# Performance work log

Hardware: AMD Instinct MI355X
Metric: run time of the kernel (lower is better)

The kernel has to match this reference:

```python
import jax, jax.numpy as jnp
import numpy as np

B, S, D = 16, 2048, 128

def setup_inputs() -> dict:
    key = jax.random.key(0)
    kq, kk, kv, km = jax.random.split(key, 4)
    Q = jax.random.normal(kq, (B, S, D), dtype=jnp.float32)
    K = jax.random.normal(kk, (B, S, D), dtype=jnp.float32)
    V = jax.random.normal(kv, (B, S, D), dtype=jnp.float32)
    # mask: True entries are masked out (filled with -inf), same as torch.masked_fill_
    mask = jax.random.randint(km, (B, S, S), 0, 2).astype(bool)
    return {"Q": Q, "K": K, "V": V, "mask": mask, "dk": 128}

def reference(Q, K, V, mask, dk):
    # scores: [B, S_q, S_k]
    w = jnp.einsum('bqd,bkd->bqk', Q, K)
    w = jnp.where(mask, -jnp.inf, w)
    # scale applied to masked scores (as in original: mask first, then divide);
    # -inf / scale stays -inf, so math matches exactly.
    scale = jnp.asarray(dk, w.dtype) ** 0.5
    p = jax.nn.softmax(w / scale, axis=-1)
    # context: [B, S_q, D]
    return jnp.einsum('bqk,bkd->bqd', p, V)
```

## Files before the change

kernel.cpp:

```cpp
#include <hip/hip_runtime.h>
#include <hip/hip_bf16.h>
#include <stdint.h>

typedef __attribute__((ext_vector_type(8)))  short short8;
typedef __attribute__((ext_vector_type(4)))  float floatx4;
typedef __attribute__((ext_vector_type(16))) float floatx16;

#define S_LEN 2048
#define DH    128
#define BQ    64
#define BKV   64
#define NSTEP (S_LEN / BKV)
#define SCALE 0.08838834764831845f
#define SCALE2 0.12753785429791905f
#define DTHR 11.541560327111708f

__device__ __forceinline__ float ex2(float x) { return __builtin_amdgcn_exp2f(x); }

__device__ __forceinline__ unsigned short f2b(float f) {
    union { float f; unsigned u; } v; v.f = f;
    unsigned r = v.u + 0x7fffu + ((v.u >> 16) & 1u);
    return (unsigned short)(r >> 16);
}

__device__ __forceinline__ unsigned cvt_pk(float lo, float hi) {
    unsigned r;
    asm("v_cvt_pk_bf16_f32 %0, %1, %2" : "=v"(r) : "v"(lo), "v"(hi));
    return r;
}

__device__ __forceinline__ void gll16(const void* g, void* l) {
    __builtin_amdgcn_global_load_lds(
        (__attribute__((address_space(1))) void*)(g),
        (__attribute__((address_space(3))) void*)(l), 16, 0, 0);
}


__global__ __launch_bounds__(256) void conv_k(const float* __restrict__ K,
                                              unsigned short* __restrict__ Kbf)
{
    int i = blockIdx.x * 256 + threadIdx.x;
    float4 v = ((const float4*)K)[i];
    ushort4 o;
    o.x = f2b(v.x); o.y = f2b(v.y); o.z = f2b(v.z); o.w = f2b(v.w);
    ((ushort4*)Kbf)[i] = o;
}

__global__ __launch_bounds__(256) void transp_v(const float* __restrict__ V,
                                                unsigned short* __restrict__ Vt)
{
    __shared__ float t[32][33];
    const int k0 = blockIdx.x * 32, d0 = blockIdx.y * 32, b = blockIdx.z;
    const int tx = threadIdx.x & 31, ty = threadIdx.x >> 5;
    const float* Vb = V + ((size_t)b * S_LEN + k0) * DH + d0;
    #pragma unroll
    for (int i = 0; i < 4; ++i)
        t[ty + 8 * i][tx] = Vb[(size_t)(ty + 8 * i) * DH + tx];
    __syncthreads();
    unsigned short* Vtb = Vt + ((size_t)b * DH + d0) * S_LEN + k0;
    #pragma unroll
    for (int i = 0; i < 4; ++i)
        Vtb[(size_t)(ty + 8 * i) * S_LEN + tx] = f2b(t[tx][ty + 8 * i]);
}

#define LDS_BYTES 69632

__global__ __launch_bounds__(256, 2)
void attn_fwd(const float* __restrict__ Q, const unsigned short* __restrict__ Kbf,
              const unsigned short* __restrict__ Vt, const int* __restrict__ M,
              float* __restrict__ O)
{
    __shared__ __align__(128) char lds[LDS_BYTES];

    const int tid  = threadIdx.x;
    const int lane = tid & 63;
    const int w    = tid >> 6;
    const int wq   = w & 1;
    const int wk   = w >> 1;
    const int lq   = lane & 31;
    const int hi   = lane >> 5;
    const int qt   = blockIdx.x;
    const int b    = blockIdx.y;
    const int q0   = qt * BQ;

    const int vd = tid & 127;
    const int vh = tid >> 7;
    const int krow_l = lane >> 4;
    const int kcol_l = (lane & 15) * 16;

    short8 qf[8];
    {
        const float* qrow = Q + ((size_t)(b * S_LEN + q0 + wq * 32 + lq)) * DH;
        #pragma unroll
        for (int dsub = 0; dsub < 8; ++dsub) {
            const float* p = qrow + dsub * 16 + hi * 8;
            float4 a  = *(const float4*)(p);
            float4 bb = *(const float4*)(p + 4);
            short8 f;
            f[0] = f2b(a.x * SCALE2);  f[1] = f2b(a.y * SCALE2);
            f[2] = f2b(a.z * SCALE2);  f[3] = f2b(a.w * SCALE2);
            f[4] = f2b(bb.x * SCALE2); f[5] = f2b(bb.y * SCALE2);
            f[6] = f2b(bb.z * SCALE2); f[7] = f2b(bb.w * SCALE2);
            qf[dsub] = f;
        }
    }

    float m_run = -1e30f;
    float l_run = 0.f;
    floatx16 accO[4];
    #pragma unroll
    for (int i = 0; i < 4; ++i) accO[i] = (floatx16)(0.f);

    const char*           Kb8 = (const char*)(Kbf + (size_t)b * S_LEN * DH);
    const unsigned short* Vtb = Vt + (size_t)b * DH * S_LEN;
    const int* Mrow = M + (size_t)b * S_LEN * S_LEN
                        + (size_t)(q0 + wq * 32 + lq) * S_LEN + wk * 32 + 4 * hi;

    short8 vreg[4];
    int4   mcur[4];

#define LOAD_MASK(TT) {                                                       \
    const int* mp_ = Mrow + (TT) * BKV;                                       \
    mcur[0] = *(const int4*)(mp_);                                            \
    mcur[1] = *(const int4*)(mp_ + 8);                                        \
    mcur[2] = *(const int4*)(mp_ + 16);                                       \
    mcur[3] = *(const int4*)(mp_ + 24); }

    #pragma unroll
    for (int i = 0; i < 4; ++i) {
        int j = (w << 2) | i;
        int r = 4 * j + krow_l;
        unsigned cb = (unsigned)kcol_l ^ (unsigned)((r & 15) << 4);
        gll16(Kb8 + (size_t)r * 256 + cb, lds + j * 1024);
    }
    #pragma unroll
    for (int j = 0; j < 4; ++j)
        vreg[j] = *(const short8*)(Vtb + (size_t)vd * S_LEN + vh * 32 + j * 8);
    #pragma unroll
    for (int j = 0; j < 4; ++j)
        *(short8*)(lds + 32768 + vd * 144 + vh * 64 + j * 16) = vreg[j];
    #pragma unroll
    for (int j = 0; j < 4; ++j)
        vreg[j] = *(const short8*)(Vtb + (size_t)vd * S_LEN + BKV + vh * 32 + j * 8);
    LOAD_MASK(0);
    __syncthreads();

#define STEP_BODY(T) {                                                        \
    const int pb  = (T) & 1;                                                  \
    const int kv0 = (T) * BKV;                                                \
                                                  \
    if ((T) + 1 < NSTEP) {                                                    \
        const char* Ksrc = Kb8 + (size_t)(kv0 + BKV) * 256;                   \
        char* KHn = lds + ((pb ^ 1) * 16384);                                 \
        _Pragma("unroll")                                                     \
        for (int i = 0; i < 4; ++i) {                                         \
            int j = (w << 2) | i;                                             \
            int r = 4 * j + krow_l;                                           \
            unsigned cb = (unsigned)kcol_l ^ (unsigned)((r & 15) << 4);       \
            gll16(Ksrc + (size_t)r * 256 + cb, KHn + j * 1024);               \
        }                                                                     \
    }                                                                         \
                            \
    if ((T) + 1 < NSTEP) {                                                    \
        _Pragma("unroll")                                                     \
        for (int j = 0; j < 4; ++j)                                           \
            *(short8*)(lds + 32768 + (pb ^ 1) * 18432 + vd * 144 + vh * 64    \
                       + j * 16) = vreg[j];                                   \
    }                                                                         \
    if ((T) + 2 < NSTEP) {                                                    \
        const unsigned short* vs_ = Vtb + (size_t)vd * S_LEN                  \
                                   + (kv0 + 2 * BKV) + vh * 32;               \
        _Pragma("unroll")                                                     \
        for (int j = 0; j < 4; ++j)                                           \
            vreg[j] = *(const short8*)(vs_ + j * 8);                          \
    }                                                                         \
            \
    floatx16 accS = (floatx16)(0.f);                                          \
    {                                                                         \
        const char* KHp = lds + pb * 16384;                                   \
        const int krow = wk * 32 + lq;                                        \
        const char* kbase = KHp + krow * 256;                                 \
        const unsigned ksw = (unsigned)((krow & 15) << 4);                    \
        __builtin_amdgcn_s_setprio(1);                                        \
        _Pragma("unroll")                                                     \
        for (int dsub = 0; dsub < 8; ++dsub) {                                \
            short8 kf = *(const short8*)(kbase +                              \
                ((unsigned)(dsub * 32 + hi * 16) ^ ksw));                     \
            accS = __builtin_amdgcn_mfma_f32_32x32x16_bf16(                   \
                       kf, qf[dsub], accS, 0, 0, 0);                          \
        }                                                                     \
        __builtin_amdgcn_s_setprio(0);                                        \
    }                                                                         \
      \
    float p_[16];                                                             \
    _Pragma("unroll")                                                         \
    for (int j = 0; j < 4; ++j) {                                             \
        int4 mm = mcur[j];                                                    \
        p_[4*j+0] = mm.x ? -1e30f : accS[4*j+0];                              \
        p_[4*j+1] = mm.y ? -1e30f : accS[4*j+1];                              \
        p_[4*j+2] = mm.z ? -1e30f : accS[4*j+2];                              \
        p_[4*j+3] = mm.w ? -1e30f : accS[4*j+3];                              \
    }                                                                         \
    float mx = p_[0];                                                         \
    _Pragma("unroll")                                                         \
    for (int r = 1; r < 16; ++r) mx = fmaxf(mx, p_[r]);                       \
    mx = fmaxf(mx, __shfl_xor(mx, 32));                                       \
    int need = __any(mx - m_run > DTHR);                                      \
    float corr = 1.0f;                                                        \
    if (need) {                                                               \
        float mn = fmaxf(m_run, mx);                                          \
        corr = ex2(m_run - mn);                                               \
        m_run = mn;                                                           \
    }                                                                         \
    float ts = 0.f;                                                           \
    _Pragma("unroll")                                                         \
    for (int r = 0; r < 16; ++r) { p_[r] = ex2(p_[r] - m_run); ts += p_[r]; } \
    ts += __shfl_xor(ts, 32);                                                 \
    if (need) {                                                               \
        l_run = l_run * corr + ts;                                            \
        _Pragma("unroll")                                                     \
        for (int ds = 0; ds < 4; ++ds) {                                      \
            floatx16 o = accO[ds];                                            \
            _Pragma("unroll")                                                 \
            for (int r = 0; r < 16; ++r) o[r] *= corr;                        \
            accO[ds] = o;                                                     \
        }                                                                     \
    } else {                                                                  \
        l_run += ts;                                                          \
    }                                                                         \
    if ((T) + 1 < NSTEP) LOAD_MASK((T) + 1);                                  \
              \
    short8 pf[2];                                                             \
    _Pragma("unroll")                                                         \
    for (int ks = 0; ks < 2; ++ks) {                                          \
        unsigned a01 = cvt_pk(p_[8*ks+0], p_[8*ks+1]);                        \
        unsigned a23 = cvt_pk(p_[8*ks+2], p_[8*ks+3]);                        \
        unsigned b01 = cvt_pk(p_[8*ks+4], p_[8*ks+5]);                        \
        unsigned b23 = cvt_pk(p_[8*ks+6], p_[8*ks+7]);                        \
        unsigned ta01 = (unsigned)__shfl_xor((int)a01, 32);                   \
        unsigned ta23 = (unsigned)__shfl_xor((int)a23, 32);                   \
        unsigned tb01 = (unsigned)__shfl_xor((int)b01, 32);                   \
        unsigned tb23 = (unsigned)__shfl_xor((int)b23, 32);                   \
        union { unsigned u[4]; short8 v; } pu;                                \
        pu.u[0] = hi ? tb01 : a01;                                            \
        pu.u[1] = hi ? tb23 : a23;                                            \
        pu.u[2] = hi ? b01 : ta01;                                            \
        pu.u[3] = hi ? b23 : ta23;                                            \
        pf[ks] = pu.v;                                                        \
    }                                                                         \
           \
    {                                                                         \
        const char* VTp = lds + 32768 + pb * 18432;                           \
        __builtin_amdgcn_s_setprio(1);                                        \
        _Pragma("unroll")                                                     \
        for (int ds = 0; ds < 4; ++ds) {                                      \
            const char* vbase = VTp + (ds * 32 + lq) * 144 + wk * 64 + hi*16; \
            _Pragma("unroll")                                                 \
            for (int ks = 0; ks < 2; ++ks) {                                  \
                short8 vf = *(const short8*)(vbase + ks * 32);                \
                accO[ds] = __builtin_amdgcn_mfma_f32_32x32x16_bf16(           \
                               vf, pf[ks], accO[ds], 0, 0, 0);                \
            }                                                                 \
        }                                                                     \
        __builtin_amdgcn_s_setprio(0);                                        \
    }                                                                         \
    __syncthreads(); }

    for (int t = 0; t < NSTEP; ++t) {
        STEP_BODY(t)
    }
#undef STEP_BODY
#undef LOAD_MASK

    {
        float* mg = (float*)lds;
        const int slot = (wq * 64 + lane) * 68;
        if (wk == 1) {
            #pragma unroll
            for (int ds = 0; ds < 4; ++ds)
                #pragma unroll
                for (int rr = 0; rr < 4; ++rr) {
                    float4 v;
                    v.x = accO[ds][4*rr+0]; v.y = accO[ds][4*rr+1];
                    v.z = accO[ds][4*rr+2]; v.w = accO[ds][4*rr+3];
                    *(float4*)(mg + slot + ds * 16 + rr * 4) = v;
                }
            mg[slot + 64] = m_run;
            mg[slot + 65] = l_run;
        }
        __syncthreads();
        if (wk == 0) {
            float m1 = mg[slot + 64], l1 = mg[slot + 65];
            float m  = fmaxf(m_run, m1);
            float f0 = ex2(m_run - m), f1 = ex2(m1 - m);
            float l  = l_run * f0 + l1 * f1;
            float inv = (l > 0.f) ? 1.f / l : 0.f;
            float* Ob = O + ((size_t)(b * S_LEN + q0 + wq * 32 + lq)) * DH;
            #pragma unroll
            for (int ds = 0; ds < 4; ++ds)
                #pragma unroll
                for (int rr = 0; rr < 4; ++rr) {
                    float4 part = *(const float4*)(mg + slot + ds * 16 + rr * 4);
                    float4 ov;
                    ov.x = (accO[ds][4*rr+0] * f0 + part.x * f1) * inv;
                    ov.y = (accO[ds][4*rr+1] * f0 + part.y * f1) * inv;
                    ov.z = (accO[ds][4*rr+2] * f0 + part.z * f1) * inv;
                    ov.w = (accO[ds][4*rr+3] * f0 + part.w * f1) * inv;
                    *(float4*)(Ob + ds * 32 + 8 * rr + 4 * hi) = ov;
                }
        }
    }
}

#define FB_LDS_BYTES 77824

__global__ __launch_bounds__(256, 2)
void attn_fwd_fb(const float* __restrict__ Q, const float* __restrict__ K,
                 const float* __restrict__ V, const int* __restrict__ M,
                 float* __restrict__ O)
{
    __shared__ __align__(128) char lds[FB_LDS_BYTES];

    const int tid  = threadIdx.x;
    const int lane = tid & 63;
    const int w    = tid >> 6;
    const int c    = lane & 15;
    const int g    = lane >> 4;
    const int qt   = blockIdx.x;
    const int b    = blockIdx.y;
    const int q0   = qt * 64;

    const int rbase = tid >> 5;
    const int c4    = tid & 31;
    const unsigned swk = (unsigned)(c4 * 8) ^ (unsigned)(rbase << 4);
    const int vd    = tid & 127;
    const int vk0   = (tid >> 7) * 32;

    short8 qf[4];
    {
        const float* qrow = Q + ((size_t)(b * S_LEN + q0 + w * 16 + c)) * DH;
        #pragma unroll
        for (int dk = 0; dk < 4; ++dk) {
            const float* p = qrow + dk * 32 + g * 8;
            float4 a  = *(const float4*)(p);
            float4 bb = *(const float4*)(p + 4);
            short8 f;
            f[0] = f2b(a.x * SCALE);  f[1] = f2b(a.y * SCALE);
            f[2] = f2b(a.z * SCALE);  f[3] = f2b(a.w * SCALE);
            f[4] = f2b(bb.x * SCALE); f[5] = f2b(bb.y * SCALE);
            f[6] = f2b(bb.z * SCALE); f[7] = f2b(bb.w * SCALE);
            qf[dk] = f;
        }
    }

    float m_run[4] = {-1e30f, -1e30f, -1e30f, -1e30f};
    float l_run[4] = {0.f, 0.f, 0.f, 0.f};
    floatx4 accO[8];
    #pragma unroll
    for (int i = 0; i < 8; ++i) accO[i] = (floatx4)(0.f);

    const float* Kb = K + (size_t)b * S_LEN * DH;
    const float* Vb = V + (size_t)b * S_LEN * DH;
    const int*   Mb = M + (size_t)b * S_LEN * S_LEN + (size_t)q0 * S_LEN;

    size_t moff[4];
    #pragma unroll
    for (int r = 0; r < 4; ++r)
        moff[r] = (size_t)(w * 16 + 4 * g + r) * S_LEN;

    float4 kreg[8];
    float  vreg[32];
    int    mreg[16];

    #pragma unroll
    for (int i = 0; i < 8; ++i)
        kreg[i] = *(const float4*)(Kb + (size_t)(i * 8 + rbase) * DH + c4 * 4);
    #pragma unroll
    for (int j = 0; j < 32; ++j)
        vreg[j] = Vb[(size_t)(vk0 + j) * DH + vd];
    #pragma unroll
    for (int r = 0; r < 4; ++r)
        #pragma unroll
        for (int n = 0; n < 4; ++n)
            mreg[r * 4 + n] = Mb[moff[r] + n * 16 + c];

    #pragma unroll
    for (int i = 0; i < 8; ++i) {
        float4 kv = kreg[i];
        unsigned long long kp =
              (unsigned long long)f2b(kv.x)
            | ((unsigned long long)f2b(kv.y) << 16)
            | ((unsigned long long)f2b(kv.z) << 32)
            | ((unsigned long long)f2b(kv.w) << 48);
        *(unsigned long long*)(lds + (i * 8 + rbase) * 256 + swk) = kp;
    }
    {
        char* vbase = lds + 32768 + vd * 144 + vk0 * 2;
        #pragma unroll
        for (int i = 0; i < 4; ++i) {
            short8 pk;
            #pragma unroll
            for (int e = 0; e < 8; ++e) pk[e] = f2b(vreg[i * 8 + e]);
            *(short8*)(vbase + i * 16) = pk;
        }
    }
    #pragma unroll
    for (int i = 0; i < 8; ++i)
        kreg[i] = *(const float4*)(Kb + (size_t)(BKV + i * 8 + rbase) * DH + c4 * 4);
    #pragma unroll
    for (int j = 0; j < 32; ++j)
        vreg[j] = Vb[(size_t)(BKV + vk0 + j) * DH + vd];

    __syncthreads();

    char* psw = lds + 69632 + w * 2048;

    for (int step = 0; step < NSTEP; ++step) {
        const int p = step & 1;
        const int kv0 = step * BKV;
        char* KHp = lds + p * 16384;
        char* VTp = lds + 32768 + p * 18432;

        floatx4 accS[4];
        #pragma unroll
        for (int n = 0; n < 4; ++n) accS[n] = (floatx4)(0.f);
        #pragma unroll
        for (int n = 0; n < 4; ++n) {
            const char* krow = KHp + (n * 16 + c) * 256;
            #pragma unroll
            for (int dk = 0; dk < 4; ++dk) {
                unsigned colb = (unsigned)(dk * 64 + g * 16) ^ (unsigned)((c & 7) << 4);
                short8 kf = *(const short8*)(krow + colb);
                accS[n] = __builtin_amdgcn_mfma_f32_16x16x32_bf16(qf[dk], kf, accS[n], 0, 0, 0);
            }
        }

        float pv[4][4];
        float corr[4];
        #pragma unroll
        for (int r = 0; r < 4; ++r) {
            float sv[4];
            #pragma unroll
            for (int n = 0; n < 4; ++n) {
                float s = accS[n][r];
                if (mreg[r * 4 + n]) s = -1e30f;
                sv[n] = s;
            }
            float tm = fmaxf(fmaxf(sv[0], sv[1]), fmaxf(sv[2], sv[3]));
            #pragma unroll
            for (int off = 1; off < 16; off <<= 1)
                tm = fmaxf(tm, __shfl_xor(tm, off, 64));
            float mn = fmaxf(m_run[r], tm);
            corr[r]  = __expf(m_run[r] - mn);
            m_run[r] = mn;
            float ts = 0.f;
            #pragma unroll
            for (int n = 0; n < 4; ++n) { pv[n][r] = __expf(sv[n] - mn); ts += pv[n][r]; }
            #pragma unroll
            for (int off = 1; off < 16; off <<= 1)
                ts += __shfl_xor(ts, off, 64);
            l_run[r] = l_run[r] * corr[r] + ts;
        }
        if (step + 1 < NSTEP) {
            const int kvn = kv0 + BKV;
            #pragma unroll
            for (int r = 0; r < 4; ++r)
                #pragma unroll
                for (int n = 0; n < 4; ++n)
                    mreg[r * 4 + n] = Mb[moff[r] + kvn + n * 16 + c];
        }

        #pragma unroll
        for (int s8 = 0; s8 < 8; ++s8) {
            floatx4 o = accO[s8];
            o[0] *= corr[0]; o[1] *= corr[1]; o[2] *= corr[2]; o[3] *= corr[3];
            accO[s8] = o;
        }

        #pragma unroll
        for (int r = 0; r < 4; ++r) {
            int rl = 4 * g + r;
            #pragma unroll
            for (int n = 0; n < 4; ++n) {
                unsigned colb = (unsigned)((n * 16 + c) * 2) ^ (unsigned)((rl & 7) << 4);
                *(unsigned short*)(psw + rl * 128 + colb) = f2b(pv[n][r]);
            }
        }

        #pragma unroll
        for (int sub = 0; sub < 2; ++sub) {
            unsigned colb = (unsigned)(sub * 64 + g * 16) ^ (unsigned)((c & 7) << 4);
            short8 pf = *(const short8*)(psw + c * 128 + colb);
            #pragma unroll
            for (int s8 = 0; s8 < 8; ++s8) {
                short8 vf = *(const short8*)(VTp + (s8 * 16 + c) * 144 + sub * 64 + g * 16);
                accO[s8] = __builtin_amdgcn_mfma_f32_16x16x32_bf16(pf, vf, accO[s8], 0, 0, 0);
            }
        }

        if (step + 1 < NSTEP) {
            char* KHn = lds + (p ^ 1) * 16384;
            char* VTn = lds + 32768 + (p ^ 1) * 18432;
            #pragma unroll
            for (int i = 0; i < 8; ++i) {
                float4 kv = kreg[i];
                unsigned long long kp =
                      (unsigned long long)f2b(kv.x)
                    | ((unsigned long long)f2b(kv.y) << 16)
                    | ((unsigned long long)f2b(kv.z) << 32)
                    | ((unsigned long long)f2b(kv.w) << 48);
                *(unsigned long long*)(KHn + (i * 8 + rbase) * 256 + swk) = kp;
            }
            char* vbase = VTn + vd * 144 + vk0 * 2;
            #pragma unroll
            for (int i = 0; i < 4; ++i) {
                short8 pk;
                #pragma unroll
                for (int e = 0; e < 8; ++e) pk[e] = f2b(vreg[i * 8 + e]);
                *(short8*)(vbase + i * 16) = pk;
            }
            if (step + 2 < NSTEP) {
                const int kvn2 = kv0 + 2 * BKV;
                #pragma unroll
                for (int i = 0; i < 8; ++i)
                    kreg[i] = *(const float4*)(Kb + (size_t)(kvn2 + i * 8 + rbase) * DH + c4 * 4);
                #pragma unroll
                for (int j = 0; j < 32; ++j)
                    vreg[j] = Vb[(size_t)(kvn2 + vk0 + j) * DH + vd];
            }
        }
        __syncthreads();
    }

    float inv[4];
    #pragma unroll
    for (int r = 0; r < 4; ++r) inv[r] = (l_run[r] > 0.f) ? 1.f / l_run[r] : 0.f;
    float* Ob = O + ((size_t)(b * S_LEN + q0 + w * 16)) * DH;
    #pragma unroll
    for (int s8 = 0; s8 < 8; ++s8) {
        #pragma unroll
        for (int r = 0; r < 4; ++r) {
            Ob[(size_t)(4 * g + r) * DH + s8 * 16 + c] = accO[s8][r] * inv[r];
        }
    }
}

extern "C" void kernel_launch(void* const* d_in, const int* in_sizes, int n_in,
                              void* d_out, int out_size, void* d_ws, size_t ws_size,
                              hipStream_t stream) {
    const float* Q = (const float*)d_in[0];
    const float* K = (const float*)d_in[1];
    const float* V = (const float*)d_in[2];
    const int*   M = (const int*)d_in[3];
    float*       O = (float*)d_out;

    const size_t elems = (size_t)16 * S_LEN * DH;
    if (ws_size >= 2 * elems * sizeof(unsigned short)) {
        unsigned short* Kbf = (unsigned short*)d_ws;
        unsigned short* Vt  = (unsigned short*)d_ws + elems;
        conv_k<<<dim3((unsigned)(elems / 4 / 256)), dim3(256), 0, stream>>>(K, Kbf);
        transp_v<<<dim3(S_LEN / 32, DH / 32, 16), dim3(256), 0, stream>>>(V, Vt);
        attn_fwd<<<dim3(S_LEN / BQ, 16), dim3(256), 0, stream>>>(Q, Kbf, Vt, M, O);
    } else {
        attn_fwd_fb<<<dim3(S_LEN / 64, 16), dim3(256), 0, stream>>>(Q, K, V, M, O);
    }
}
```

Before: 118.5 us.

## Pre-pack attention mask into bitmasks via ballot before the attention kernel

Adds a pack_mask kernel that reads the int32 mask once and uses wave ballots to compress it into 64-bit bitmasks, 32 words per query row. The attention kernel then reads those bitmasks instead of 16-byte int vectors per step, and double-buffers one group of four KV steps ahead. This cuts the mask traffic and register pressure inside the compute-bound attention loop. The cost is an extra kernel launch and serialising the full mask read ahead of attention instead of overlapping it. It also needs more workspace, and the slow fallback path runs if that workspace is missing.

```diff
diff --git a/kernel.cpp b/kernel.cpp
--- a/kernel.cpp
+++ b/kernel.cpp
@@ -63,11 +63,36 @@
         Vtb[(size_t)(ty + 8 * i) * S_LEN + tx] = f2b(t[tx][ty + 8 * i]);
 }
 
+__global__ __launch_bounds__(256) void pack_mask(const int* __restrict__ M,
+                                                 unsigned long long* __restrict__ P)
+{
+    const int lane = threadIdx.x & 63;
+    const int wv   = threadIdx.x >> 6;
+    const int row  = blockIdx.x * 4 + wv;
+    const int* Mr  = M + (size_t)row * S_LEN;
+    unsigned long long* Pr = P + (size_t)row * 32;
+    #pragma unroll
+    for (int it = 0; it < 8; ++it) {
+        int4 v = *(const int4*)(Mr + it * 256 + lane * 4);
+        unsigned long long b0 = __ballot(v.x != 0);
+        unsigned long long b1 = __ballot(v.y != 0);
+        unsigned long long b2 = __ballot(v.z != 0);
+        unsigned long long b3 = __ballot(v.w != 0);
+        if (lane == 0) {
+            Pr[it * 4 + 0] = b0;
+            Pr[it * 4 + 1] = b1;
+            Pr[it * 4 + 2] = b2;
+            Pr[it * 4 + 3] = b3;
+        }
+    }
+}
+
 #define LDS_BYTES 69632
 
 __global__ __launch_bounds__(256, 2)
 void attn_fwd(const float* __restrict__ Q, const unsigned short* __restrict__ Kbf,
-              const unsigned short* __restrict__ Vt, const int* __restrict__ M,
+              const unsigned short* __restrict__ Vt,
+              const unsigned long long* __restrict__ Pm,
               float* __restrict__ O)
 {
     __shared__ __align__(128) char lds[LDS_BYTES];
@@ -113,18 +138,16 @@
 
     const char*           Kb8 = (const char*)(Kbf + (size_t)b * S_LEN * DH);
     const unsigned short* Vtb = Vt + (size_t)b * DH * S_LEN;
-    const int* Mrow = M + (size_t)b * S_LEN * S_LEN
-                        + (size_t)(q0 + wq * 32 + lq) * S_LEN + wk * 32 + 4 * hi;
+    const unsigned long long* Pk = Pm
+        + ((size_t)(b * S_LEN + q0 + wq * 32 + lq) << 5);
 
     short8 vreg[4];
-    int4   mcur[4];
-
-#define LOAD_MASK(TT) {                                                       \
-    const int* mp_ = Mrow + (TT) * BKV;                                       \
-    mcur[0] = *(const int4*)(mp_);                                            \
-    mcur[1] = *(const int4*)(mp_ + 8);                                        \
-    mcur[2] = *(const int4*)(mp_ + 16);                                       \
-    mcur[3] = *(const int4*)(mp_ + 24); }
+    unsigned long long mgc[4], mgn[4];
+
+#define LOAD_MG(DST, G) {                                                     \
+    ulonglong2 a_ = *(const ulonglong2*)(Pk + (G) * 4);                       \
+    ulonglong2 b_ = *(const ulonglong2*)(Pk + (G) * 4 + 2);                   \
+    DST[0] = a_.x; DST[1] = a_.y; DST[2] = b_.x; DST[3] = b_.y; }
 
     #pragma unroll
     for (int i = 0; i < 4; ++i) {
@@ -142,10 +165,11 @@
     #pragma unroll
     for (int j = 0; j < 4; ++j)
         vreg[j] = *(const short8*)(Vtb + (size_t)vd * S_LEN + BKV + vh * 32 + j * 8);
-    LOAD_MASK(0);
+    LOAD_MG(mgc, 0);
+    LOAD_MG(mgn, 1);
     __syncthreads();
 
-#define STEP_BODY(T) {                                                        \
+#define STEP_BODY(T, TT) {                                                    \
     const int pb  = (T) & 1;                                                  \
     const int kv0 = (T) * BKV;                                                \
                                                   \
@@ -191,15 +215,19 @@
         }                                                                     \
         __builtin_amdgcn_s_setprio(0);                                        \
     }                                                                         \
-      \
+                               \
+    const int base_ = (TT) * 16 + wk * 8 + hi;                                \
+    unsigned mb0 = (unsigned)(mgc[0] >> base_);                               \
+    unsigned mb1 = (unsigned)(mgc[1] >> base_);                               \
+    unsigned mb2 = (unsigned)(mgc[2] >> base_);                               \
+    unsigned mb3 = (unsigned)(mgc[3] >> base_);                               \
     float p_[16];                                                             \
     _Pragma("unroll")                                                         \
     for (int j = 0; j < 4; ++j) {                                             \
-        int4 mm = mcur[j];                                                    \
-        p_[4*j+0] = mm.x ? -1e30f : accS[4*j+0];                              \
-        p_[4*j+1] = mm.y ? -1e30f : accS[4*j+1];                              \
-        p_[4*j+2] = mm.z ? -1e30f : accS[4*j+2];                              \
-        p_[4*j+3] = mm.w ? -1e30f : accS[4*j+3];                              \
+        p_[4*j+0] = ((mb0 >> (2*j)) & 1u) ? -1e30f : accS[4*j+0];             \
+        p_[4*j+1] = ((mb1 >> (2*j)) & 1u) ? -1e30f : accS[4*j+1];             \
+        p_[4*j+2] = ((mb2 >> (2*j)) & 1u) ? -1e30f : accS[4*j+2];             \
+        p_[4*j+3] = ((mb3 >> (2*j)) & 1u) ? -1e30f : accS[4*j+3];             \
     }                                                                         \
     float mx = p_[0];                                                         \
     _Pragma("unroll")                                                         \
@@ -228,7 +256,6 @@
     } else {                                                                  \
         l_run += ts;                                                          \
     }                                                                         \
-    if ((T) + 1 < NSTEP) LOAD_MASK((T) + 1);                                  \
               \
     short8 pf[2];                                                             \
     _Pragma("unroll")                                                         \
@@ -266,11 +293,16 @@
     }                                                                         \
     __syncthreads(); }
 
-    for (int t = 0; t < NSTEP; ++t) {
-        STEP_BODY(t)
+    for (int g = 0; g < 8; ++g) {
+        STEP_BODY(4 * g + 0, 0)
+        STEP_BODY(4 * g + 1, 1)
+        STEP_BODY(4 * g + 2, 2)
+        STEP_BODY(4 * g + 3, 3)
+        mgc[0] = mgn[0]; mgc[1] = mgn[1]; mgc[2] = mgn[2]; mgc[3] = mgn[3];
+        if (g + 2 < 8) LOAD_MG(mgn, g + 2);
     }
 #undef STEP_BODY
-#undef LOAD_MASK
+#undef LOAD_MG
 
     {
         float* mg = (float*)lds;
@@ -554,13 +586,17 @@
     const int*   M = (const int*)d_in[3];
     float*       O = (float*)d_out;
 
-    const size_t elems = (size_t)16 * S_LEN * DH;
-    if (ws_size >= 2 * elems * sizeof(unsigned short)) {
-        unsigned short* Kbf = (unsigned short*)d_ws;
-        unsigned short* Vt  = (unsigned short*)d_ws + elems;
+    const size_t elems    = (size_t)16 * S_LEN * DH;
+    const size_t kv_bytes = elems * sizeof(unsigned short);
+    const size_t pm_bytes = (size_t)16 * S_LEN * 32 * 8;
+    if (ws_size >= 2 * kv_bytes + pm_bytes) {
+        unsigned short*     Kbf = (unsigned short*)d_ws;
+        unsigned short*     Vt  = (unsigned short*)d_ws + elems;
+        unsigned long long* Pm  = (unsigned long long*)((char*)d_ws + 2 * kv_bytes);
         conv_k<<<dim3((unsigned)(elems / 4 / 256)), dim3(256), 0, stream>>>(K, Kbf);
         transp_v<<<dim3(S_LEN / 32, DH / 32, 16), dim3(256), 0, stream>>>(V, Vt);
-        attn_fwd<<<dim3(S_LEN / BQ, 16), dim3(256), 0, stream>>>(Q, Kbf, Vt, M, O);
+        pack_mask<<<dim3(16 * S_LEN / 4), dim3(256), 0, stream>>>(M, Pm);
+        attn_fwd<<<dim3(S_LEN / BQ, 16), dim3(256), 0, stream>>>(Q, Kbf, Vt, Pm, O);
     } else {
         attn_fwd_fb<<<dim3(S_LEN / 64, 16), dim3(256), 0, stream>>>(Q, K, V, M, O);
     }
```

Result: slower. 136.6 us (+15.3%).
